# Performance work log

Hardware: AMD Instinct MI355X
Metric: run time of the kernel (lower is better)

The kernel has to match this reference:

```python
import jax, jax.numpy as jnp
import numpy as np

F_DIM = 128; T = 3; N_RBF = 20; CUTOFF = 5.0; EPS = 1e-8
N_ATOMS = 10000; N_EDGES = 320000; N_MOL = 16; MAX_Z = 100


def setup_inputs():
    key = jax.random.key(0)
    ks = jax.random.split(key, 30)
    def w(k, shape, fan_in):
        return (jax.random.normal(k, shape, dtype=jnp.float32) / np.float32(np.sqrt(fan_in)))
    inp = {}
    inp["atomic_numbers"] = jax.random.randint(ks[0], (N_ATOMS,), 1, MAX_Z)
    inp["r_ij"] = jax.random.normal(ks[1], (N_EDGES, 3), dtype=jnp.float32) * 1.5
    inp["idx_i"] = jax.random.randint(ks[2], (N_EDGES,), 0, N_ATOMS)
    inp["idx_j"] = jax.random.randint(ks[3], (N_EDGES,), 0, N_ATOMS)
    inp["idx_m"] = jnp.sort(jax.random.randint(ks[4], (N_ATOMS,), 0, N_MOL))
    inp["e_field"] = jax.random.normal(ks[5], (N_MOL, 3), dtype=jnp.float32) * 0.1
    emb = jax.random.normal(ks[6], (MAX_Z, F_DIM), dtype=jnp.float32)
    inp["emb"] = emb.at[0].set(0.0)  # padding_idx=0
    inp["filt_W"] = w(ks[7], (N_RBF, T * 3 * F_DIM), N_RBF)
    inp["filt_b"] = jnp.zeros((T * 3 * F_DIM,), jnp.float32)
    inp["inter_W1"] = w(ks[8], (T, F_DIM, F_DIM), F_DIM)
    inp["inter_b1"] = jnp.zeros((T, F_DIM), jnp.float32)
    inp["inter_W2"] = w(ks[9], (T, F_DIM, 3 * F_DIM), F_DIM)
    inp["inter_b2"] = jnp.zeros((T, 3 * F_DIM), jnp.float32)
    inp["field_sW1"] = w(ks[10], (T, F_DIM, F_DIM), F_DIM)
    inp["field_sb1"] = jnp.zeros((T, F_DIM), jnp.float32)
    inp["field_sW2"] = w(ks[11], (T, F_DIM, F_DIM), F_DIM)
    inp["field_sb2"] = jnp.zeros((T, F_DIM), jnp.float32)
    inp["field_vW"] = w(ks[12], (T, F_DIM, F_DIM), F_DIM)
    inp["mix_muW"] = w(ks[13], (T, F_DIM, 2 * F_DIM), F_DIM)
    inp["mix_W1"] = w(ks[14], (T, 2 * F_DIM, F_DIM), 2 * F_DIM)
    inp["mix_b1"] = jnp.zeros((T, F_DIM), jnp.float32)
    inp["mix_W2"] = w(ks[15], (T, F_DIM, 3 * F_DIM), F_DIM)
    inp["mix_b2"] = jnp.zeros((T, 3 * F_DIM), jnp.float32)
    return inp


def _forward(r_ij, e_field, emb, filt_W, filt_b, inter_W1, inter_b1, inter_W2, inter_b2,
             field_sW1, field_sb1, field_sW2, field_sb2, field_vW,
             mix_muW, mix_W1, mix_b1, mix_W2, mix_b2,
             atomic_numbers, idx_i, idx_j, idx_m):
    silu = jax.nn.silu
    n_atoms = atomic_numbers.shape[0]
    # distances / directions
    d = jnp.sqrt(jnp.sum(r_ij * r_ij, axis=1, keepdims=True))        # [E,1]
    dir_ij = r_ij / d                                                # [E,3]
    # Gaussian RBF expansion
    offsets = jnp.linspace(0.0, CUTOFF, N_RBF, dtype=jnp.float32)
    width = offsets[1] - offsets[0]
    phi = jnp.exp(-0.5 * ((d[..., None] - offsets) / width) ** 2)    # [E,1,n_rbf]
    # cosine cutoff
    fcut = 0.5 * (jnp.cos(d * jnp.pi / CUTOFF) + 1.0) * (d < CUTOFF) # [E,1]
    filters = (phi @ filt_W + filt_b) * fcut[..., None]              # [E,1,T*3F]
    filter_list = jnp.split(filters, T, axis=-1)                     # T x [E,1,3F]
    q = emb[atomic_numbers][:, None, :]                              # [N,1,F]
    mu = jnp.zeros((n_atoms, 3, F_DIM), dtype=q.dtype)               # [N,3,F]
    E = e_field[idx_m][..., None]                                    # [N,3,1]
    for t in range(T):
        # --- PaiNNInteraction: edge message passing ---
        x = silu(q @ inter_W1[t] + inter_b1[t]) @ inter_W2[t] + inter_b2[t]  # [N,1,3F]
        xj = x[idx_j]                                                # [E,1,3F]
        muj = mu[idx_j]                                              # [E,3,F]
        xx = filter_list[t] * xj                                     # [E,1,3F]
        dq_e, dmuR, dmumu = jnp.split(xx, 3, axis=-1)                # [E,1,F] each
        dq = jax.ops.segment_sum(dq_e[:, 0, :], idx_i, num_segments=n_atoms)[:, None, :]
        dmu_e = dmuR * dir_ij[:, :, None] + dmumu * muj              # [E,3,F]
        dmu = jax.ops.segment_sum(dmu_e, idx_i, num_segments=n_atoms)
        q = q + dq
        mu = mu + dmu
        # --- FieldInteraction: pseudo-polarizability coupling ---
        a_s = silu(q @ field_sW1[t] + field_sb1[t]) @ field_sW2[t] + field_sb2[t]  # [N,1,F]
        a_v = mu @ field_vW[t]                                       # [N,3,F]
        mu = mu + a_s * E - jnp.sum(a_v * E, axis=1, keepdims=True) * a_v
        # --- PaiNNMixing: intra-atomic scalar/vector mixing ---
        mu_mix = mu @ mix_muW[t]                                     # [N,3,2F]
        mu_V, mu_Wc = jnp.split(mu_mix, 2, axis=-1)                  # [N,3,F]
        mu_Vn = jnp.sqrt(jnp.sum(mu_V ** 2, axis=-2, keepdims=True) + EPS)  # [N,1,F]
        ctx = jnp.concatenate([q, mu_Vn], axis=-1)                   # [N,1,2F]
        y = silu(ctx @ mix_W1[t] + mix_b1[t]) @ mix_W2[t] + mix_b2[t]  # [N,1,3F]
        dq_i, dmu_i, dqmu_i = jnp.split(y, 3, axis=-1)
        q = q + dq_i + dqmu_i * jnp.sum(mu_V * mu_Wc, axis=1, keepdims=True)
        mu = mu + dmu_i * mu_Wc
    # pack scalar (q [N,1,F]) and vector (mu [N,3,F]) reps into [N,4,F]
    return jnp.concatenate([q, mu], axis=1)


def reference(atomic_numbers, r_ij, idx_i, idx_j, idx_m, e_field, emb, filt_W, filt_b,
              inter_W1, inter_b1, inter_W2, inter_b2,
              field_sW1, field_sb1, field_sW2, field_sb2, field_vW,
              mix_muW, mix_W1, mix_b1, mix_W2, mix_b2):
    return _forward(r_ij, e_field, emb, filt_W, filt_b, inter_W1, inter_b1, inter_W2, inter_b2,
                    field_sW1, field_sb1, field_sW2, field_sb2, field_vW,
                    mix_muW, mix_W1, mix_b1, mix_W2, mix_b2,
                    atomic_numbers, idx_i, idx_j, idx_m)
```

## Files before the change

### kernel.cpp

```cpp
#include <hip/hip_runtime.h>

#define NA 10000
#define NE 320000

typedef short short8 __attribute__((ext_vector_type(8)));
typedef unsigned short us4 __attribute__((ext_vector_type(4)));
typedef float f32x4 __attribute__((ext_vector_type(4)));

__device__ __forceinline__ float silu_f(float v) { return v / (1.0f + __expf(-v)); }

__device__ __forceinline__ void split_bf16(float x, unsigned short& h, unsigned short& l)
{
    unsigned int u = __float_as_uint(x);
    h = (unsigned short)(u >> 16);
    float hf = __uint_as_float((unsigned int)h << 16);
    unsigned int ul = __float_as_uint(x - hf) + 0x8000u;
    l = (unsigned short)(ul >> 16);
}

__global__ __launch_bounds__(256) void k_init(
    const int* __restrict__ Z, const int* __restrict__ idx_m,
    const float* __restrict__ emb, const float* __restrict__ e_field,
    float* __restrict__ q, float* __restrict__ mu,
    float* __restrict__ Eat, int* __restrict__ counts, int* __restrict__ cursor)
{
    int gid = blockIdx.x * 256 + threadIdx.x;
    if (gid < NA * 384) mu[gid] = 0.0f;
    if (gid < NA * 128) {
        int i = gid >> 7, f = gid & 127;
        q[gid] = emb[Z[i] * 128 + f];
    }
    if (gid < NA * 3) {
        int i = gid / 3, d = gid - i * 3;
        Eat[gid] = e_field[idx_m[i] * 3 + d];
    }
    if (gid < NA) { counts[gid] = 0; cursor[gid] = 0; }
}

__global__ __launch_bounds__(256) void k_count(
    const int* __restrict__ idx_i, int* __restrict__ counts)
{
    int e = blockIdx.x * 256 + threadIdx.x;
    if (e < NE) atomicAdd(&counts[idx_i[e]], 1);
}

__global__ __launch_bounds__(256) void k_scan(const int* __restrict__ counts,
                                              int* __restrict__ rowptr)
{
    __shared__ int part[256];
    int tid = threadIdx.x;
    const int CH = (NA + 255) / 256;
    int base = tid * CH;
    int s = 0;
    for (int i2 = 0; i2 < CH; i2++) {
        int idx = base + i2;
        if (idx < NA) s += counts[idx];
    }
    part[tid] = s;
    __syncthreads();
    for (int ofs = 1; ofs < 256; ofs <<= 1) {
        int v = part[tid];
        int add = (tid >= ofs) ? part[tid - ofs] : 0;
        __syncthreads();
        part[tid] = v + add;
        __syncthreads();
    }
    int run = (tid > 0) ? part[tid - 1] : 0;
    for (int i2 = 0; i2 < CH; i2++) {
        int idx = base + i2;
        if (idx < NA) { rowptr[idx] = run; run += counts[idx]; }
        else if (idx == NA) rowptr[NA] = run;
    }
}

__global__ __launch_bounds__(256) void k_geom_scatter(
    const float* __restrict__ r_ij, const int* __restrict__ idx_i,
    const int* __restrict__ idx_j, const int* __restrict__ rowptr,
    int* __restrict__ cursor, float* __restrict__ phi_s,
    float4* __restrict__ df_s, int* __restrict__ j_s)
{
    int e = blockIdx.x * 256 + threadIdx.x;
    if (e >= NE) return;
    float x = r_ij[e*3+0], y = r_ij[e*3+1], z = r_ij[e*3+2];
    float d = sqrtf(x*x + y*y + z*z);
    float inv = 1.0f / d;
    float fc = (d < 5.0f) ? 0.5f * (__cosf(d * 0.628318530717958648f) + 1.0f) : 0.0f;
    int i = idx_i[e];
    int pos = rowptr[i] + atomicAdd(&cursor[i], 1);
    float4 dv; dv.x = x*inv; dv.y = y*inv; dv.z = z*inv; dv.w = fc;
    df_s[pos] = dv;
    j_s[pos] = idx_j[e];
    const float invw = 19.0f / 5.0f;
    float ph[20];
    #pragma unroll
    for (int k = 0; k < 20; k++) {
        float off = (5.0f / 19.0f) * (float)k;
        float u = (d - off) * invw;
        ph[k] = __expf(-0.5f * u * u) * fc;
    }
    #pragma unroll
    for (int c = 0; c < 5; c++) {
        float4 pv; pv.x = ph[c*4]; pv.y = ph[c*4+1]; pv.z = ph[c*4+2]; pv.w = ph[c*4+3];
        *(float4*)(phi_s + (size_t)pos*20 + c*4) = pv;
    }
}

struct WDesc { const float* src; unsigned short* dh; unsigned short* dl; int K; int N; };
struct WPack { WDesc w[24]; };

__global__ __launch_bounds__(256) void k_wprep(WPack P)
{
    WDesc d = P.w[blockIdx.y];
    int kBlks = d.K >> 5, nStrips = d.N >> 4;
    int total = nStrips * kBlks * 64;
    int g = blockIdx.x * 256 + threadIdx.x;
    if (g >= total) return;
    int lane = g & 63, rem = g >> 6;
    int kb = rem % kBlks, sIdx = rem / kBlks;
    int m16 = lane & 15, quad = lane >> 4;
    int n = sIdx * 16 + m16;
    int kbase = kb * 32 + quad * 8;
    size_t dofs = (size_t)g * 8;
    #pragma unroll
    for (int jj = 0; jj < 8; jj++) {
        unsigned short h, l;
        split_bf16(d.src[(size_t)(kbase + jj) * d.N + n], h, l);
        d.dh[dofs + jj] = h;
        d.dl[dofs + jj] = l;
    }
}

template<int ACT>
__global__ __launch_bounds__(256) void k_gmm2(
    const float* __restrict__ A,
    const unsigned short* __restrict__ Bh, const unsigned short* __restrict__ Bl,
    const float* __restrict__ bias, float* __restrict__ C,
    int M, int K, int N)
{
    __shared__ unsigned short Ahs[64 * 40];
    __shared__ unsigned short Als[64 * 40];
    int tid = threadIdx.x, lane = tid & 63, wv = tid >> 6;
    int i0 = blockIdx.x * 64, n0 = blockIdx.y * 64;
    int m16 = lane & 15, quad = lane >> 4;
    int kBlks = K >> 5;
    int sIdx = blockIdx.y * 4 + wv;

    f32x4 acc[4];
    #pragma unroll
    for (int a = 0; a < 4; a++) acc[a] = 0.0f;

    for (int kb = 0; kb < kBlks; kb++) {
        int k0 = kb << 5;
        __syncthreads();
        #pragma unroll
        for (int s = 0; s < 2; s++) {
            int idx = s * 256 + tid;
            int r = idx >> 3, c4 = (idx & 7) << 2;
            float4 v = {0.f, 0.f, 0.f, 0.f};
            if (i0 + r < M) v = *(const float4*)(A + (size_t)(i0 + r) * K + k0 + c4);
            unsigned short h0,l0,h1,l1,h2,l2,h3,l3;
            split_bf16(v.x, h0, l0); split_bf16(v.y, h1, l1);
            split_bf16(v.z, h2, l2); split_bf16(v.w, h3, l3);
            us4 hv = {h0, h1, h2, h3}, lv = {l0, l1, l2, l3};
            *(us4*)(Ahs + r * 40 + c4) = hv;
            *(us4*)(Als + r * 40 + c4) = lv;
        }
        __syncthreads();
        size_t bofs = (((size_t)sIdx * kBlks + kb) * 64 + lane) * 8;
        short8 bh = *(const short8*)(Bh + bofs);
        short8 bl = *(const short8*)(Bl + bofs);
        #pragma unroll
        for (int tm = 0; tm < 4; tm++) {
            short8 ah = *(const short8*)(Ahs + (tm * 16 + m16) * 40 + quad * 8);
            short8 al = *(const short8*)(Als + (tm * 16 + m16) * 40 + quad * 8);
            acc[tm] = __builtin_amdgcn_mfma_f32_16x16x32_bf16(ah, bh, acc[tm], 0, 0, 0);
            acc[tm] = __builtin_amdgcn_mfma_f32_16x16x32_bf16(ah, bl, acc[tm], 0, 0, 0);
            acc[tm] = __builtin_amdgcn_mfma_f32_16x16x32_bf16(al, bh, acc[tm], 0, 0, 0);
        }
    }
    int col = n0 + wv * 16 + m16;
    float bv = bias ? bias[col] : 0.0f;
    #pragma unroll
    for (int tm = 0; tm < 4; tm++) {
        #pragma unroll
        for (int r = 0; r < 4; r++) {
            int row = i0 + tm * 16 + quad * 4 + r;
            if (row < M) {
                float v = acc[tm][r] + bv;
                if (ACT) v = silu_f(v);
                C[(size_t)row * N + col] = v;
            }
        }
    }
}

__global__ __launch_bounds__(256, 3) void k_edge4(
    int t, const float* __restrict__ phi_s, const float4* __restrict__ df_s,
    const int* __restrict__ j_s, const int* __restrict__ rowptr,
    const float* __restrict__ x, const float* __restrict__ mu_in,
    const float* __restrict__ filt_W, const float* __restrict__ filt_b,
    float* __restrict__ q, float* __restrict__ mu_out)
{
    int lane = threadIdx.x & 63;
    int wv   = threadIdx.x >> 6;
    int ia   = blockIdx.x * 2 + (wv >> 1);
    int h    = wv & 1;
    int f    = lane + h * 64;

    float wreg[3][20];
    float b3[3];
    #pragma unroll
    for (int c = 0; c < 3; c++) {
        int col = t * 384 + (2*c + h) * 64 + lane;
        b3[c] = filt_b[col];
        #pragma unroll
        for (int k = 0; k < 20; k++)
            wreg[c][k] = filt_W[k * 1152 + col];
    }

    float accq = 0.0f, acc0 = 0.0f, acc1 = 0.0f, acc2 = 0.0f;
    int p0 = rowptr[ia], p1 = rowptr[ia + 1];
    int p = p0;
    for (; p + 4 <= p1; p += 4) {
        int jj[4]; float4 df[4];
        #pragma unroll
        for (int e = 0; e < 4; e++) { jj[e] = j_s[p + e]; df[e] = df_s[p + e]; }
        float dots[4][3];
        #pragma unroll
        for (int e = 0; e < 4; e++)
            #pragma unroll
            for (int c = 0; c < 3; c++) dots[e][c] = df[e].w * b3[c];
        #pragma unroll
        for (int kq = 0; kq < 5; kq++) {
            float4 a[4];
            #pragma unroll
            for (int e = 0; e < 4; e++)
                a[e] = *(const float4*)(phi_s + (size_t)(p + e) * 20 + kq * 4);
            #pragma unroll
            for (int e = 0; e < 4; e++) {
                #pragma unroll
                for (int c = 0; c < 3; c++) {
                    dots[e][c] = fmaf(a[e].x, wreg[c][kq*4+0], dots[e][c]);
                    dots[e][c] = fmaf(a[e].y, wreg[c][kq*4+1], dots[e][c]);
                    dots[e][c] = fmaf(a[e].z, wreg[c][kq*4+2], dots[e][c]);
                    dots[e][c] = fmaf(a[e].w, wreg[c][kq*4+3], dots[e][c]);
                }
            }
        }
        float xv[4][3], mv[4][3];
        #pragma unroll
        for (int e = 0; e < 4; e++) {
            size_t xb = (size_t)jj[e] * 384;
            xv[e][0] = x[xb + h*64 + lane];
            xv[e][1] = x[xb + (2+h)*64 + lane];
            xv[e][2] = x[xb + (4+h)*64 + lane];
            #pragma unroll
            for (int d = 0; d < 3; d++)
                mv[e][d] = mu_in[((size_t)jj[e]*3 + d)*128 + f];
        }
        #pragma unroll
        for (int e = 0; e < 4; e++) {
            float xxq = dots[e][0] * xv[e][0];
            float xxr = dots[e][1] * xv[e][1];
            float xxm = dots[e][2] * xv[e][2];
            accq += xxq;
            acc0 += xxr * df[e].x + xxm * mv[e][0];
            acc1 += xxr * df[e].y + xxm * mv[e][1];
            acc2 += xxr * df[e].z + xxm * mv[e][2];
        }
    }
    for (; p < p1; p++) {
        int j0 = j_s[p];
        float4 d0 = df_s[p];
        float dots0[3];
        #pragma unroll
        for (int c = 0; c < 3; c++) dots0[c] = d0.w * b3[c];
        #pragma unroll
        for (int kq = 0; kq < 5; kq++) {
            float4 a0 = *(const float4*)(phi_s + (size_t)p * 20 + kq * 4);
            #pragma unroll
            for (int c = 0; c < 3; c++) {
                dots0[c] = fmaf(a0.x, wreg[c][kq*4+0], dots0[c]);
                dots0[c] = fmaf(a0.y, wreg[c][kq*4+1], dots0[c]);
                dots0[c] = fmaf(a0.z, wreg[c][kq*4+2], dots0[c]);
                dots0[c] = fmaf(a0.w, wreg[c][kq*4+3], dots0[c]);
            }
        }
        size_t xb = (size_t)j0 * 384;
        float xq0 = x[xb + h*64 + lane];
        float xr0 = x[xb + (2+h)*64 + lane];
        float xm0 = x[xb + (4+h)*64 + lane];
        float m00 = mu_in[((size_t)j0*3 + 0)*128 + f];
        float m01 = mu_in[((size_t)j0*3 + 1)*128 + f];
        float m02 = mu_in[((size_t)j0*3 + 2)*128 + f];
        float xxq0 = dots0[0] * xq0, xxr0 = dots0[1] * xr0, xxm0 = dots0[2] * xm0;
        accq += xxq0;
        acc0 += xxr0*d0.x + xxm0*m00;
        acc1 += xxr0*d0.y + xxm0*m01;
        acc2 += xxr0*d0.z + xxm0*m02;
    }
    q[(size_t)ia*128 + f] += accq;
    mu_out[((size_t)ia*3 + 0)*128 + f] = mu_in[((size_t)ia*3 + 0)*128 + f] + acc0;
    mu_out[((size_t)ia*3 + 1)*128 + f] = mu_in[((size_t)ia*3 + 1)*128 + f] + acc1;
    mu_out[((size_t)ia*3 + 2)*128 + f] = mu_in[((size_t)ia*3 + 2)*128 + f] + acc2;
}

__global__ __launch_bounds__(256) void k_field(
    const float* __restrict__ a_s, const float* __restrict__ av,
    const float* __restrict__ Eat, float* __restrict__ mu)
{
    int gid = blockIdx.x * 256 + threadIdx.x;
    if (gid >= NA * 128) return;
    int i = gid >> 7, f = gid & 127;
    float E0 = Eat[i*3+0], E1 = Eat[i*3+1], E2 = Eat[i*3+2];
    float a0 = av[(i*3+0)*128+f], a1 = av[(i*3+1)*128+f], a2 = av[(i*3+2)*128+f];
    float dot = a0*E0 + a1*E1 + a2*E2;
    float s = a_s[gid];
    mu[(i*3+0)*128+f] += s*E0 - dot*a0;
    mu[(i*3+1)*128+f] += s*E1 - dot*a1;
    mu[(i*3+2)*128+f] += s*E2 - dot*a2;
}

__global__ __launch_bounds__(256) void k_mixnorm(
    const float* __restrict__ q, const float* __restrict__ mumix,
    float* __restrict__ ctx)
{
    int gid = blockIdx.x * 256 + threadIdx.x;
    if (gid >= NA * 128) return;
    int i = gid >> 7, f = gid & 127;
    float v0 = mumix[(i*3+0)*256+f], v1 = mumix[(i*3+1)*256+f], v2 = mumix[(i*3+2)*256+f];
    float vn = sqrtf(v0*v0 + v1*v1 + v2*v2 + 1e-8f);
    ctx[i*256 + f]       = q[gid];
    ctx[i*256 + 128 + f] = vn;
}

__global__ __launch_bounds__(256) void k_mixupd(
    const float* __restrict__ y, const float* __restrict__ mumix,
    float* __restrict__ q, float* __restrict__ mu)
{
    int gid = blockIdx.x * 256 + threadIdx.x;
    if (gid >= NA * 128) return;
    int i = gid >> 7, f = gid & 127;
    float yq  = y[i*384 + f];
    float ym  = y[i*384 + 128 + f];
    float yqm = y[i*384 + 256 + f];
    float sdot = 0.f;
    #pragma unroll
    for (int d = 0; d < 3; d++)
        sdot += mumix[(i*3+d)*256 + f] * mumix[(i*3+d)*256 + 128 + f];
    q[gid] += yq + yqm * sdot;
    #pragma unroll
    for (int d = 0; d < 3; d++)
        mu[(i*3+d)*128 + f] += ym * mumix[(i*3+d)*256 + 128 + f];
}

__global__ __launch_bounds__(256) void k_pack(
    const float* __restrict__ q, const float* __restrict__ mu,
    float* __restrict__ out)
{
    int gid = blockIdx.x * 256 + threadIdx.x;
    if (gid >= NA * 512) return;
    int i = gid >> 9, c = gid & 511;
    out[gid] = (c < 128) ? q[i*128 + c] : mu[i*384 + (c - 128)];
}

extern "C" void kernel_launch(void* const* d_in, const int* in_sizes, int n_in,
                              void* d_out, int out_size, void* d_ws, size_t ws_size,
                              hipStream_t stream)
{
    const int*   Z       = (const int*)d_in[0];
    const float* r_ij    = (const float*)d_in[1];
    const int*   idx_i   = (const int*)d_in[2];
    const int*   idx_j   = (const int*)d_in[3];
    const int*   idx_m   = (const int*)d_in[4];
    const float* e_field = (const float*)d_in[5];
    const float* emb     = (const float*)d_in[6];
    const float* filt_W  = (const float*)d_in[7];
    const float* filt_b  = (const float*)d_in[8];
    const float* iW1     = (const float*)d_in[9];
    const float* ib1     = (const float*)d_in[10];
    const float* iW2     = (const float*)d_in[11];
    const float* ib2     = (const float*)d_in[12];
    const float* sW1     = (const float*)d_in[13];
    const float* sb1     = (const float*)d_in[14];
    const float* sW2     = (const float*)d_in[15];
    const float* sb2     = (const float*)d_in[16];
    const float* vW      = (const float*)d_in[17];
    const float* mmW     = (const float*)d_in[18];
    const float* mW1     = (const float*)d_in[19];
    const float* mb1     = (const float*)d_in[20];
    const float* mW2     = (const float*)d_in[21];
    const float* mb2     = (const float*)d_in[22];
    float* out = (float*)d_out;

    float* base = (float*)d_ws;
    size_t off = 0;
    auto alloc = [&](size_t n) { float* p = base + off; off += (n + 255) & ~(size_t)255; return p; };
    float* q     = alloc((size_t)NA*128);
    float* mu_a  = alloc((size_t)NA*384);
    float* mu_b  = alloc((size_t)NA*384);
    float* h     = alloc((size_t)NA*128);
    float* a_s   = alloc((size_t)NA*128);
    float* s384  = alloc((size_t)NA*384);
    float* mumix = alloc((size_t)NA*768);
    float* ctx   = alloc((size_t)NA*256);
    float* Eat   = alloc((size_t)NA*3);
    float* phi_s = alloc((size_t)NE*20);
    float4* df_s = (float4*)alloc((size_t)NE*4);
    int* rowptr  = (int*)alloc(NA + 1);
    int* counts  = (int*)alloc(NA);
    int* cursor  = (int*)alloc(NA);
    int* j_s     = (int*)alloc(NE);
    unsigned short* wth = (unsigned short*)alloc(344064 + 256);
    unsigned short* wtl = (unsigned short*)alloc(344064 + 256);
    (void)ws_size; (void)in_sizes; (void)n_in; (void)out_size;

    WPack P;
    size_t woff = 0;
    unsigned short* WH[3][8];
    unsigned short* WL[3][8];
    int nw = 0;
    auto reg = [&](const float* src, int K, int N, int t, int slot) {
        P.w[nw].src = src; P.w[nw].dh = wth + woff; P.w[nw].dl = wtl + woff;
        P.w[nw].K = K; P.w[nw].N = N;
        WH[t][slot] = wth + woff; WL[t][slot] = wtl + woff;
        woff += (size_t)K * N; nw++;
    };
    for (int t = 0; t < 3; t++) {
        reg(iW1 + t*128*128, 128, 128, t, 0);
        reg(iW2 + t*128*384, 128, 384, t, 1);
        reg(sW1 + t*128*128, 128, 128, t, 2);
        reg(sW2 + t*128*128, 128, 128, t, 3);
        reg(vW  + t*128*128, 128, 128, t, 4);
        reg(mmW + t*128*256, 128, 256, t, 5);
        reg(mW1 + t*256*128, 256, 128, t, 6);
        reg(mW2 + t*128*384, 128, 384, t, 7);
    }

    k_wprep       <<<dim3(24, 24),          256, 0, stream>>>(P);
    k_init        <<<(NA*384 + 255)/256,    256, 0, stream>>>(Z, idx_m, emb, e_field, q, mu_a, Eat, counts, cursor);
    k_count       <<<(NE + 255)/256,        256, 0, stream>>>(idx_i, counts);
    k_scan        <<<1,                     256, 0, stream>>>(counts, rowptr);
    k_geom_scatter<<<(NE + 255)/256,        256, 0, stream>>>(r_ij, idx_i, idx_j, rowptr, cursor,
                                                              phi_s, df_s, j_s);

    const int G64  = (NA + 63) / 64;
    const int G64x3 = (NA*3 + 63) / 64;
    float* mu_cur = mu_a;
    float* mu_nxt = mu_b;
    for (int t = 0; t < 3; t++) {
        k_gmm2<1><<<dim3(G64, 2),   256, 0, stream>>>(q, WH[t][0], WL[t][0], ib1 + t*128, h,    NA, 128, 128);
        k_gmm2<0><<<dim3(G64, 6),   256, 0, stream>>>(h, WH[t][1], WL[t][1], ib2 + t*384, s384, NA, 128, 384);
        k_edge4<<<NA/2, 256, 0, stream>>>(t, phi_s, df_s, j_s, rowptr, s384,
                                          mu_cur, filt_W, filt_b, q, mu_nxt);
        { float* tmp = mu_cur; mu_cur = mu_nxt; mu_nxt = tmp; }
        k_gmm2<1><<<dim3(G64, 2),   256, 0, stream>>>(q,      WH[t][2], WL[t][2], sb1 + t*128, h,    NA,   128, 128);
        k_gmm2<0><<<dim3(G64, 2),   256, 0, stream>>>(h,      WH[t][3], WL[t][3], sb2 + t*128, a_s,  NA,   128, 128);
        k_gmm2<0><<<dim3(G64x3, 2), 256, 0, stream>>>(mu_cur, WH[t][4], WL[t][4], nullptr,     s384, NA*3, 128, 128);
        k_field<<<(NA*128 + 255)/256, 256, 0, stream>>>(a_s, s384, Eat, mu_cur);
        k_gmm2<0><<<dim3(G64x3, 4), 256, 0, stream>>>(mu_cur, WH[t][5], WL[t][5], nullptr,     mumix, NA*3, 128, 256);
        k_mixnorm<<<(NA*128 + 255)/256, 256, 0, stream>>>(q, mumix, ctx);
        k_gmm2<1><<<dim3(G64, 2),   256, 0, stream>>>(ctx,    WH[t][6], WL[t][6], mb1 + t*128, h,    NA, 256, 128);
        k_gmm2<0><<<dim3(G64, 6),   256, 0, stream>>>(h,      WH[t][7], WL[t][7], mb2 + t*384, s384, NA, 128, 384);
        k_mixupd<<<(NA*128 + 255)/256, 256, 0, stream>>>(s384, mumix, q, mu_cur);
    }
    k_pack<<<(NA*512 + 255)/256, 256, 0, stream>>>(q, mu_cur, out);
}
```

Before: 1.116 ms.

## Fuse two-layer MLPs into one kernel and split edge loop across two wave pairs

Adds a k_mlp kernel that computes silu(A@W1+b1)@W2+b2 for a 32-row tile, keeping the hidden activation in shared memory as split bf16 instead of writing it to global memory. It replaces three pairs of GEMM launches per interaction step. The edge kernel now assigns one atom per block and splits its neighbour list between two wave pairs, combining partial sums through shared memory. This doubles parallelism on the edge phase and raises occupancy bounds. The cost is smaller row tiles in the MLP, weight reloads per block, and an extra barrier in the edge kernel.

```diff
diff --git a/kernel.cpp b/kernel.cpp
--- a/kernel.cpp
+++ b/kernel.cpp
@@ -194,17 +194,138 @@
     }
 }
 
-__global__ __launch_bounds__(256, 3) void k_edge4(
+template<int K1, int N2>
+__global__ __launch_bounds__(256, 2) void k_mlp(
+    const float* __restrict__ A,
+    const unsigned short* __restrict__ B1h, const unsigned short* __restrict__ B1l,
+    const float* __restrict__ b1,
+    const unsigned short* __restrict__ B2h, const unsigned short* __restrict__ B2l,
+    const float* __restrict__ b2, float* __restrict__ C, int M)
+{
+    const int KB1 = K1 / 32;
+    const int S2  = N2 / 64;
+    __shared__ unsigned short A1h[32 * 40];
+    __shared__ unsigned short A1l[32 * 40];
+    __shared__ unsigned short Hh[32 * 136];
+    __shared__ unsigned short Hl[32 * 136];
+
+    int tid = threadIdx.x, lane = tid & 63, wv = tid >> 6;
+    int i0 = blockIdx.x * 32;
+    int m16 = lane & 15, quad = lane >> 4;
+
+    f32x4 acc1[2][2];
+    #pragma unroll
+    for (int s = 0; s < 2; s++)
+        #pragma unroll
+        for (int tm = 0; tm < 2; tm++) acc1[s][tm] = 0.0f;
+
+    for (int kb = 0; kb < KB1; kb++) {
+        int k0 = kb << 5;
+        __syncthreads();
+        {
+            int r = tid >> 3, c4 = (tid & 7) << 2;
+            float4 v = {0.f, 0.f, 0.f, 0.f};
+            if (i0 + r < M) v = *(const float4*)(A + (size_t)(i0 + r) * K1 + k0 + c4);
+            unsigned short h0,l0,h1,l1,h2,l2,h3,l3;
+            split_bf16(v.x, h0, l0); split_bf16(v.y, h1, l1);
+            split_bf16(v.z, h2, l2); split_bf16(v.w, h3, l3);
+            us4 hv = {h0, h1, h2, h3}, lv = {l0, l1, l2, l3};
+            *(us4*)(A1h + r * 40 + c4) = hv;
+            *(us4*)(A1l + r * 40 + c4) = lv;
+        }
+        __syncthreads();
+        #pragma unroll
+        for (int tm = 0; tm < 2; tm++) {
+            short8 ah = *(const short8*)(A1h + (tm * 16 + m16) * 40 + quad * 8);
+            short8 al = *(const short8*)(A1l + (tm * 16 + m16) * 40 + quad * 8);
+            #pragma unroll
+            for (int s = 0; s < 2; s++) {
+                int sIdx = wv * 2 + s;
+                size_t bofs = (((size_t)sIdx * KB1 + kb) * 64 + lane) * 8;
+                short8 bh = *(const short8*)(B1h + bofs);
+                short8 bl = *(const short8*)(B1l + bofs);
+                acc1[s][tm] = __builtin_amdgcn_mfma_f32_16x16x32_bf16(ah, bh, acc1[s][tm], 0, 0, 0);
+                acc1[s][tm] = __builtin_amdgcn_mfma_f32_16x16x32_bf16(ah, bl, acc1[s][tm], 0, 0, 0);
+                acc1[s][tm] = __builtin_amdgcn_mfma_f32_16x16x32_bf16(al, bh, acc1[s][tm], 0, 0, 0);
+            }
+        }
+    }
+    __syncthreads();
+    #pragma unroll
+    for (int s = 0; s < 2; s++) {
+        int col = wv * 32 + s * 16 + m16;
+        float bb = b1[col];
+        #pragma unroll
+        for (int tm = 0; tm < 2; tm++) {
+            #pragma unroll
+            for (int r = 0; r < 4; r++) {
+                int row = tm * 16 + quad * 4 + r;
+                float v = silu_f(acc1[s][tm][r] + bb);
+                unsigned short h, l;
+                split_bf16(v, h, l);
+                Hh[row * 136 + col] = h;
+                Hl[row * 136 + col] = l;
+            }
+        }
+    }
+    __syncthreads();
+
+    f32x4 acc2[S2][2];
+    #pragma unroll
+    for (int s = 0; s < S2; s++)
+        #pragma unroll
+        for (int tm = 0; tm < 2; tm++) acc2[s][tm] = 0.0f;
+
+    #pragma unroll
+    for (int kb = 0; kb < 4; kb++) {
+        short8 ah[2], al[2];
+        #pragma unroll
+        for (int tm = 0; tm < 2; tm++) {
+            ah[tm] = *(const short8*)(Hh + (tm * 16 + m16) * 136 + kb * 32 + quad * 8);
+            al[tm] = *(const short8*)(Hl + (tm * 16 + m16) * 136 + kb * 32 + quad * 8);
+        }
+        #pragma unroll
+        for (int s = 0; s < S2; s++) {
+            int sIdx = wv * S2 + s;
+            size_t bofs = (((size_t)sIdx * 4 + kb) * 64 + lane) * 8;
+            short8 bh = *(const short8*)(B2h + bofs);
+            short8 bl = *(const short8*)(B2l + bofs);
+            #pragma unroll
+            for (int tm = 0; tm < 2; tm++) {
+                acc2[s][tm] = __builtin_amdgcn_mfma_f32_16x16x32_bf16(ah[tm], bh, acc2[s][tm], 0, 0, 0);
+                acc2[s][tm] = __builtin_amdgcn_mfma_f32_16x16x32_bf16(ah[tm], bl, acc2[s][tm], 0, 0, 0);
+                acc2[s][tm] = __builtin_amdgcn_mfma_f32_16x16x32_bf16(al[tm], bh, acc2[s][tm], 0, 0, 0);
+            }
+        }
+    }
+    #pragma unroll
+    for (int s = 0; s < S2; s++) {
+        int col = (wv * S2 + s) * 16 + m16;
+        float bb = b2 ? b2[col] : 0.0f;
+        #pragma unroll
+        for (int tm = 0; tm < 2; tm++) {
+            #pragma unroll
+            for (int r = 0; r < 4; r++) {
+                int row = i0 + tm * 16 + quad * 4 + r;
+                if (row < M) C[(size_t)row * N2 + col] = acc2[s][tm][r] + bb;
+            }
+        }
+    }
+}
+
+__global__ __launch_bounds__(256, 4) void k_edge5(
     int t, const float* __restrict__ phi_s, const float4* __restrict__ df_s,
     const int* __restrict__ j_s, const int* __restrict__ rowptr,
     const float* __restrict__ x, const float* __restrict__ mu_in,
     const float* __restrict__ filt_W, const float* __restrict__ filt_b,
     float* __restrict__ q, float* __restrict__ mu_out)
 {
+    __shared__ float comb[2][4][64];
     int lane = threadIdx.x & 63;
     int wv   = threadIdx.x >> 6;
-    int ia   = blockIdx.x * 2 + (wv >> 1);
     int h    = wv & 1;
+    int seg  = wv >> 1;
+    int ia   = blockIdx.x;
     int f    = lane + h * 64;
 
     float wreg[3][20];
@@ -218,10 +339,15 @@
             wreg[c][k] = filt_W[k * 1152 + col];
     }
 
+    int p0 = rowptr[ia], p1 = rowptr[ia + 1];
+    int n = p1 - p0;
+    int half = (n + 1) >> 1;
+    int ps = seg ? (p0 + half) : p0;
+    int pe = seg ? p1 : (p0 + half);
+
     float accq = 0.0f, acc0 = 0.0f, acc1 = 0.0f, acc2 = 0.0f;
-    int p0 = rowptr[ia], p1 = rowptr[ia + 1];
-    int p = p0;
-    for (; p + 4 <= p1; p += 4) {
+    int p = ps;
+    for (; p + 4 <= pe; p += 4) {
         int jj[4]; float4 df[4];
         #pragma unroll
         for (int e = 0; e < 4; e++) { jj[e] = j_s[p + e]; df[e] = df_s[p + e]; }
@@ -269,7 +395,7 @@
             acc2 += xxr * df[e].z + xxm * mv[e][2];
         }
     }
-    for (; p < p1; p++) {
+    for (; p < pe; p++) {
         int j0 = j_s[p];
         float4 d0 = df_s[p];
         float dots0[3];
@@ -299,10 +425,23 @@
         acc1 += xxr0*d0.y + xxm0*m01;
         acc2 += xxr0*d0.z + xxm0*m02;
     }
-    q[(size_t)ia*128 + f] += accq;
-    mu_out[((size_t)ia*3 + 0)*128 + f] = mu_in[((size_t)ia*3 + 0)*128 + f] + acc0;
-    mu_out[((size_t)ia*3 + 1)*128 + f] = mu_in[((size_t)ia*3 + 1)*128 + f] + acc1;
-    mu_out[((size_t)ia*3 + 2)*128 + f] = mu_in[((size_t)ia*3 + 2)*128 + f] + acc2;
+    if (seg == 1) {
+        comb[h][0][lane] = accq;
+        comb[h][1][lane] = acc0;
+        comb[h][2][lane] = acc1;
+        comb[h][3][lane] = acc2;
+    }
+    __syncthreads();
+    if (seg == 0) {
+        accq += comb[h][0][lane];
+        acc0 += comb[h][1][lane];
+        acc1 += comb[h][2][lane];
+        acc2 += comb[h][3][lane];
+        q[(size_t)ia*128 + f] += accq;
+        mu_out[((size_t)ia*3 + 0)*128 + f] = mu_in[((size_t)ia*3 + 0)*128 + f] + acc0;
+        mu_out[((size_t)ia*3 + 1)*128 + f] = mu_in[((size_t)ia*3 + 1)*128 + f] + acc1;
+        mu_out[((size_t)ia*3 + 2)*128 + f] = mu_in[((size_t)ia*3 + 2)*128 + f] + acc2;
+    }
 }
 
 __global__ __launch_bounds__(256) void k_field(
@@ -399,7 +538,6 @@
     float* q     = alloc((size_t)NA*128);
     float* mu_a  = alloc((size_t)NA*384);
     float* mu_b  = alloc((size_t)NA*384);
-    float* h     = alloc((size_t)NA*128);
     float* a_s   = alloc((size_t)NA*128);
     float* s384  = alloc((size_t)NA*384);
     float* mumix = alloc((size_t)NA*768);
@@ -444,24 +582,24 @@
     k_geom_scatter<<<(NE + 255)/256,        256, 0, stream>>>(r_ij, idx_i, idx_j, rowptr, cursor,
                                                               phi_s, df_s, j_s);
 
-    const int G64  = (NA + 63) / 64;
+    const int G32   = (NA + 31) / 32;
     const int G64x3 = (NA*3 + 63) / 64;
     float* mu_cur = mu_a;
     float* mu_nxt = mu_b;
     for (int t = 0; t < 3; t++) {
-        k_gmm2<1><<<dim3(G64, 2),   256, 0, stream>>>(q, WH[t][0], WL[t][0], ib1 + t*128, h,    NA, 128, 128);
-        k_gmm2<0><<<dim3(G64, 6),   256, 0, stream>>>(h, WH[t][1], WL[t][1], ib2 + t*384, s384, NA, 128, 384);
-        k_edge4<<<NA/2, 256, 0, stream>>>(t, phi_s, df_s, j_s, rowptr, s384,
-                                          mu_cur, filt_W, filt_b, q, mu_nxt);
+        k_mlp<128,384><<<G32, 256, 0, stream>>>(q, WH[t][0], WL[t][0], ib1 + t*128,
+                                                WH[t][1], WL[t][1], ib2 + t*384, s384, NA);
+        k_edge5<<<NA, 256, 0, stream>>>(t, phi_s, df_s, j_s, rowptr, s384,
+                                        mu_cur, filt_W, filt_b, q, mu_nxt);
         { float* tmp = mu_cur; mu_cur = mu_nxt; mu_nxt = tmp; }
-        k_gmm2<1><<<dim3(G64, 2),   256, 0, stream>>>(q,      WH[t][2], WL[t][2], sb1 + t*128, h,    NA,   128, 128);
-        k_gmm2<0><<<dim3(G64, 2),   256, 0, stream>>>(h,      WH[t][3], WL[t][3], sb2 + t*128, a_s,  NA,   128, 128);
-        k_gmm2<0><<<dim3(G64x3, 2), 256, 0, stream>>>(mu_cur, WH[t][4], WL[t][4], nullptr,     s384, NA*3, 128, 128);
+        k_mlp<128,128><<<G32, 256, 0, stream>>>(q, WH[t][2], WL[t][2], sb1 + t*128,
+                                                WH[t][3], WL[t][3], sb2 + t*128, a_s, NA);
+        k_gmm2<0><<<dim3(G64x3, 2), 256, 0, stream>>>(mu_cur, WH[t][4], WL[t][4], nullptr, s384, NA*3, 128, 128);
         k_field<<<(NA*128 + 255)/256, 256, 0, stream>>>(a_s, s384, Eat, mu_cur);
-        k_gmm2<0><<<dim3(G64x3, 4), 256, 0, stream>>>(mu_cur, WH[t][5], WL[t][5], nullptr,     mumix, NA*3, 128, 256);
+        k_gmm2<0><<<dim3(G64x3, 4), 256, 0, stream>>>(mu_cur, WH[t][5], WL[t][5], nullptr, mumix, NA*3, 128, 256);
         k_mixnorm<<<(NA*128 + 255)/256, 256, 0, stream>>>(q, mumix, ctx);
-        k_gmm2<1><<<dim3(G64, 2),   256, 0, stream>>>(ctx,    WH[t][6], WL[t][6], mb1 + t*128, h,    NA, 256, 128);
-        k_gmm2<0><<<dim3(G64, 6),   256, 0, stream>>>(h,      WH[t][7], WL[t][7], mb2 + t*384, s384, NA, 128, 384);
+        k_mlp<256,384><<<G32, 256, 0, stream>>>(ctx, WH[t][6], WL[t][6], mb1 + t*128,
+                                                WH[t][7], WL[t][7], mb2 + t*384, s384, NA);
         k_mixupd<<<(NA*128 + 255)/256, 256, 0, stream>>>(s384, mumix, q, mu_cur);
     }
     k_pack<<<(NA*512 + 255)/256, 256, 0, stream>>>(q, mu_cur, out);
```

Result: slower. 1.397 ms (+25.1%).
